# Optimization experiments

Measured on AMD Instinct MI355X. Metric: run time of the kernel, lower is better.

## Reference

```python
import jax, jax.numpy as jnp
import numpy as np
import math

HEADS = 4
LN_EPS = 1e-5


def _layer_norm(x, gamma, beta):
    # LayerNorm over last dim (N=4096), matching nn.LayerNorm(4096)
    mu = jnp.mean(x, axis=-1, keepdims=True)
    var = jnp.mean((x - mu) ** 2, axis=-1, keepdims=True)
    return (x - mu) * jax.lax.rsqrt(var + LN_EPS) * gamma + beta


def setup_inputs() -> dict:
    key = jax.random.key(0)
    ks = jax.random.split(key, 10)
    L, IMG, N = 1024, 1024, 4096
    s_img = 1.0 / math.sqrt(IMG)
    s_L = 1.0 / math.sqrt(L)
    return {
        "point_features": jax.random.normal(ks[0], (1, L, N), jnp.float32),
        "img_features": jax.random.normal(ks[1], (1, IMG, N), jnp.float32),
        # 4 per-head 1x1 convs IMG_chl -> L_chl
        "W_img": jax.random.normal(ks[2], (HEADS, L, IMG), jnp.float32) * s_img,
        "b_img": jax.random.normal(ks[3], (HEADS, L), jnp.float32) * s_img,
        # conv_L: L_chl -> L_chl
        "W_L": jax.random.normal(ks[4], (L, L), jnp.float32) * s_L,
        "b_L": jax.random.normal(ks[5], (L,), jnp.float32) * s_L,
        # LayerNorm(4096)
        "ln_g": jnp.ones((N,), jnp.float32),
        "ln_b": jnp.zeros((N,), jnp.float32),
        # conv_fusion: L_chl -> L_chl
        "W_f": jax.random.normal(ks[6], (L, L), jnp.float32) * s_L,
        "b_f": jax.random.normal(ks[7], (L,), jnp.float32) * s_L,
    }


def reference(point_features, img_features, W_img, b_img, W_L, b_L, ln_g, ln_b, W_f, b_f):
    # L_query = conv_L(point_features): [1, L, N]
    L_query = jnp.einsum('oi,bin->bon', W_L, point_features) + b_L[None, :, None]
    dk = L_query.shape[1]
    N = L_query.shape[2]

    # All 4 head keys at once: [H, 1, L, N]
    keys = jnp.einsum('hoi,bin->hbon', W_img, img_features) + b_img[:, None, :, None]

    # score_i = sum_c(key_i * query) / sqrt(dk)  -> cat over heads: [H, N] (B=1)
    score = jnp.sum(keys * L_query[None], axis=2).reshape(HEADS, N) / jnp.sqrt(jnp.float32(dk))

    # softmax across heads (dim=0), weightmap = [1, H, N]
    weight = jax.nn.softmax(score, axis=0)
    weightmap = weight[None]

    # z = sum_h weight[h] * key_h : [1, L, N]
    z = jnp.einsum('hn,hbcn->bcn', weight, keys)

    fused = _layer_norm(z + L_query, ln_g, ln_b)
    fusion_features = jnp.einsum('oi,bin->bon', W_f, fused) + b_f[None, :, None]
    return (fusion_features, weightmap)
```

## Files before the change

kernel.cpp:

```cpp
#include <hip/hip_runtime.h>
#include <hip/hip_bf16.h>
#include <stdint.h>

using u16 = unsigned short;

typedef __attribute__((ext_vector_type(8))) short bf16x8;
typedef __attribute__((ext_vector_type(4))) float f32x4;

typedef const __attribute__((address_space(1))) unsigned int* gas_t;
typedef __attribute__((address_space(3))) unsigned int* las_t;

__device__ inline void g2l16(const u16* g, u16* l) {
  __builtin_amdgcn_global_load_lds((gas_t)g, (las_t)l, 16, 0, 0);
}

__device__ inline u16 f2b(float x) {
  union { float f; uint32_t u; } v; v.f = x;
  uint32_t r = (v.u + 0x7FFFu + ((v.u >> 16) & 1u)) >> 16;
  return (u16)r;
}
__device__ inline float b2f(u16 b) {
  union { uint32_t u; float f; } v; v.u = ((uint32_t)b) << 16;
  return v.f;
}
__device__ inline float b2f_lo(uint32_t p) {
  union { uint32_t u; float f; } v; v.u = p << 16; return v.f;
}
__device__ inline float b2f_hi(uint32_t p) {
  union { uint32_t u; float f; } v; v.u = p & 0xFFFF0000u; return v.f;
}

__device__ inline void store_out(float* p, float v) { *p = v; }
__device__ inline void store_out(u16* p, float v) { *p = f2b(v); }

template<typename OutT>
__device__ inline void gemm_tile_128(const u16* __restrict__ A,
                                     const u16* __restrict__ Bt,
                                     const float* __restrict__ bias,
                                     OutT* __restrict__ C,
                                     int m0, int n0, int N, int K,
                                     u16* As, u16* Bs)
{
  const int tid  = threadIdx.x;
  const int wave = tid >> 6;
  const int lane = tid & 63;
  const int wm = wave >> 1, wn = wave & 1;
  const int lr = lane & 15;
  const int lq = lane >> 4;
  const int x7 = lr & 7;

  const int srow = tid >> 3;
  const int sgc  = (tid & 7) ^ (srow & 7);
  const u16* gA = A  + (size_t)(m0 + srow) * K + sgc * 8;
  const u16* gB = Bt + (size_t)(n0 + srow) * K + sgc * 8;
  u16* dstA = As + wave * 512;
  u16* dstB = Bs + wave * 512;

  f32x4 acc[4][4];
  #pragma unroll
  for (int i = 0; i < 4; ++i)
    #pragma unroll
    for (int j = 0; j < 4; ++j)
      acc[i][j] = (f32x4){0.f, 0.f, 0.f, 0.f};

  for (int k0 = 0; k0 < K; k0 += 64) {
    #pragma unroll
    for (int s = 0; s < 4; ++s) {
      g2l16(gA + (size_t)(s * 32) * K + k0, dstA + s * 2048);
      g2l16(gB + (size_t)(s * 32) * K + k0, dstB + s * 2048);
    }
    __syncthreads();

    #pragma unroll
    for (int ks = 0; ks < 2; ++ks) {
      const int pa = (ks * 4 + lq) ^ x7;
      bf16x8 af[4], bfr[4];
      #pragma unroll
      for (int im = 0; im < 4; ++im)
        af[im] = *(const bf16x8*)&As[(wm * 64 + im * 16 + lr) * 64 + pa * 8];
      #pragma unroll
      for (int in = 0; in < 4; ++in)
        bfr[in] = *(const bf16x8*)&Bs[(wn * 64 + in * 16 + lr) * 64 + pa * 8];

      #pragma unroll
      for (int im = 0; im < 4; ++im)
        #pragma unroll
        for (int in = 0; in < 4; ++in)
          acc[im][in] = __builtin_amdgcn_mfma_f32_16x16x32_bf16(
              af[im], bfr[in], acc[im][in], 0, 0, 0);
    }
    __syncthreads();
  }

  #pragma unroll
  for (int im = 0; im < 4; ++im) {
    const int mbase = m0 + wm * 64 + im * 16 + lq * 4;
    #pragma unroll
    for (int in = 0; in < 4; ++in) {
      const int ncol = n0 + wn * 64 + in * 16 + lr;
      #pragma unroll
      for (int r = 0; r < 4; ++r) {
        const int m = mbase + r;
        store_out(C + (size_t)m * N + ncol, acc[im][in][r] + bias[m]);
      }
    }
  }
}

__global__ __launch_bounds__(256)
void gemm_keys_q(const u16* __restrict__ WIb, const u16* __restrict__ IT,
                 const float* __restrict__ bim, u16* __restrict__ KEYS,
                 const u16* __restrict__ WLb, const u16* __restrict__ PT,
                 const float* __restrict__ bL, u16* __restrict__ Qb)
{
  __shared__ u16 As[128 * 64];
  __shared__ u16 Bs[128 * 64];
  const int by = blockIdx.y;
  const bool keys = (by < 32);
  const u16*   A    = keys ? WIb : WLb;
  const u16*   Bt   = keys ? IT  : PT;
  const float* bias = keys ? bim : bL;
  u16*         C    = keys ? KEYS : Qb;
  const int m0 = (by & 31) * 128;
  const int n0 = blockIdx.x * 128;
  gemm_tile_128<u16>(A, Bt, bias, C, m0, n0, 4096, 1024, As, Bs);
}

template<typename OutT>
__global__ __launch_bounds__(256)
void gemm_bt_64(const u16* __restrict__ A, const u16* __restrict__ Bt,
                const float* __restrict__ bias, OutT* __restrict__ C,
                int M, int N, int K)
{
  __shared__ u16 As[64 * 64];
  __shared__ u16 Bs[128 * 64];

  const int tid  = threadIdx.x;
  const int wave = tid >> 6;
  const int lane = tid & 63;
  const int lr = lane & 15;
  const int lq = lane >> 4;
  const int x7 = lr & 7;

  const int m0 = blockIdx.y * 64;
  const int n0 = blockIdx.x * 128;

  const int srow = tid >> 3;
  const int sgc  = (tid & 7) ^ (srow & 7);
  const u16* gA = A  + (size_t)(m0 + srow) * K + sgc * 8;
  const u16* gB = Bt + (size_t)(n0 + srow) * K + sgc * 8;
  u16* dstA = As + wave * 512;
  u16* dstB = Bs + wave * 512;

  f32x4 acc[4][2];
  #pragma unroll
  for (int i = 0; i < 4; ++i)
    #pragma unroll
    for (int j = 0; j < 2; ++j)
      acc[i][j] = (f32x4){0.f, 0.f, 0.f, 0.f};

  for (int k0 = 0; k0 < K; k0 += 64) {
    #pragma unroll
    for (int s = 0; s < 2; ++s)
      g2l16(gA + (size_t)(s * 32) * K + k0, dstA + s * 2048);
    #pragma unroll
    for (int s = 0; s < 4; ++s)
      g2l16(gB + (size_t)(s * 32) * K + k0, dstB + s * 2048);
    __syncthreads();

    #pragma unroll
    for (int ks = 0; ks < 2; ++ks) {
      const int pa = (ks * 4 + lq) ^ x7;
      bf16x8 af[4], bfr[2];
      #pragma unroll
      for (int im = 0; im < 4; ++im)
        af[im] = *(const bf16x8*)&As[(im * 16 + lr) * 64 + pa * 8];
      #pragma unroll
      for (int in = 0; in < 2; ++in)
        bfr[in] = *(const bf16x8*)&Bs[(wave * 32 + in * 16 + lr) * 64 + pa * 8];

      #pragma unroll
      for (int im = 0; im < 4; ++im)
        #pragma unroll
        for (int in = 0; in < 2; ++in)
          acc[im][in] = __builtin_amdgcn_mfma_f32_16x16x32_bf16(
              af[im], bfr[in], acc[im][in], 0, 0, 0);
    }
    __syncthreads();
  }

  #pragma unroll
  for (int im = 0; im < 4; ++im) {
    const int mbase = m0 + im * 16 + lq * 4;
    #pragma unroll
    for (int in = 0; in < 2; ++in) {
      const int ncol = n0 + wave * 32 + in * 16 + lr;
      #pragma unroll
      for (int r = 0; r < 4; ++r) {
        const int m = mbase + r;
        store_out(C + (size_t)m * N + ncol, acc[im][in][r] + bias[m]);
      }
    }
  }
}

__device__ inline void transpose_tile_f32(const float* __restrict__ in,
                                          u16* __restrict__ out,
                                          int R, int C, int r0, int c0)
{
  __shared__ u16 T[64 * 68];
  const int tr = (threadIdx.x >> 4) * 4;
  const int tc = (threadIdx.x & 15) * 4;
  float4 v[4];
  #pragma unroll
  for (int i = 0; i < 4; ++i)
    v[i] = *(const float4*)&in[(size_t)(r0 + tr + i) * C + c0 + tc];
  #pragma unroll
  for (int j = 0; j < 4; ++j) {
    ushort4 o;
    o.x = f2b(((const float*)&v[0])[j]);
    o.y = f2b(((const float*)&v[1])[j]);
    o.z = f2b(((const float*)&v[2])[j]);
    o.w = f2b(((const float*)&v[3])[j]);
    *(ushort4*)&T[(tc + j) * 68 + tr] = o;
  }
  __syncthreads();
  #pragma unroll
  for (int j = 0; j < 4; ++j) {
    const ushort4 o = *(const ushort4*)&T[(tr + j) * 68 + tc];
    *(ushort4*)&out[(size_t)(c0 + tr + j) * R + r0 + tc] = o;
  }
}

__device__ inline void transpose_tile_u16(const u16* __restrict__ in,
                                          u16* __restrict__ out,
                                          int R, int C, int r0, int c0)
{
  __shared__ u16 T[64 * 68];
  const int tr = (threadIdx.x >> 4) * 4;
  const int tc = (threadIdx.x & 15) * 4;
  ushort4 v[4];
  #pragma unroll
  for (int i = 0; i < 4; ++i)
    v[i] = *(const ushort4*)&in[(size_t)(r0 + tr + i) * C + c0 + tc];
  #pragma unroll
  for (int j = 0; j < 4; ++j) {
    ushort4 o;
    o.x = ((const u16*)&v[0])[j];
    o.y = ((const u16*)&v[1])[j];
    o.z = ((const u16*)&v[2])[j];
    o.w = ((const u16*)&v[3])[j];
    *(ushort4*)&T[(tc + j) * 68 + tr] = o;
  }
  __syncthreads();
  #pragma unroll
  for (int j = 0; j < 4; ++j) {
    const ushort4 o = *(const ushort4*)&T[(tr + j) * 68 + tc];
    *(ushort4*)&out[(size_t)(c0 + tr + j) * R + r0 + tc] = o;
  }
}

__global__ __launch_bounds__(256)
void prep(const float* __restrict__ P, u16* __restrict__ PT,
          const float* __restrict__ I, u16* __restrict__ IT,
          const float4* __restrict__ wim, const float4* __restrict__ wl,
          const float4* __restrict__ wf, ushort4* __restrict__ wimb,
          ushort4* __restrict__ wlb, ushort4* __restrict__ wfb,
          float4* __restrict__ score0)
{
  const int bid = blockIdx.x;
  if (bid < 2048) {
    const int z   = bid >> 10;
    const int rem = bid & 1023;
    const int c0  = (rem & 63) * 64;
    const int r0  = (rem >> 6) * 64;
    transpose_tile_f32(z ? I : P, z ? IT : PT, 1024, 4096, r0, c0);
  } else if (bid < 8192) {
    int i = (bid - 2048) * 256 + threadIdx.x;
    const float4* src; ushort4* dst;
    if (i < 1048576)      { src = wim; dst = wimb; }
    else if (i < 1310720) { src = wl;  dst = wlb;  i -= 1048576; }
    else                  { src = wf;  dst = wfb;  i -= 1310720; }
    const float4 v = src[i];
    ushort4 o;
    o.x = f2b(v.x); o.y = f2b(v.y); o.z = f2b(v.z); o.w = f2b(v.w);
    dst[i] = o;
  } else {
    const int i = (bid - 8192) * 256 + threadIdx.x;
    score0[i] = (float4){0.f, 0.f, 0.f, 0.f};
  }
}

__global__ __launch_bounds__(256)
void transpose_u16(const u16* __restrict__ in, u16* __restrict__ out)
{
  const int c0 = (blockIdx.x & 63) * 64;
  const int r0 = (blockIdx.x >> 6) * 64;
  transpose_tile_u16(in, out, 1024, 4096, r0, c0);
}

__global__ __launch_bounds__(256)
void score_partial(const u16* __restrict__ keys, const u16* __restrict__ Qb,
                   float* __restrict__ score)
{
  const int n  = (blockIdx.x * 256 + threadIdx.x) * 2;
  const int c0 = blockIdx.y * 16;
  float s0[4] = {0.f, 0.f, 0.f, 0.f};
  float s1[4] = {0.f, 0.f, 0.f, 0.f};
  for (int c = c0; c < c0 + 16; ++c) {
    const uint32_t qv = *(const uint32_t*)&Qb[(size_t)c * 4096 + n];
    const float q0 = b2f_lo(qv), q1 = b2f_hi(qv);
    #pragma unroll
    for (int h = 0; h < 4; ++h) {
      const uint32_t kv = *(const uint32_t*)&keys[((size_t)((h << 10) + c)) * 4096 + n];
      s0[h] = fmaf(q0, b2f_lo(kv), s0[h]);
      s1[h] = fmaf(q1, b2f_hi(kv), s1[h]);
    }
  }
  #pragma unroll
  for (int h = 0; h < 4; ++h) {
    atomicAdd(&score[h * 4096 + n],     s0[h] * 0.03125f);
    atomicAdd(&score[h * 4096 + n + 1], s1[h] * 0.03125f);
  }
}

__global__ __launch_bounds__(256)
void softmax_h(const float* __restrict__ score, float* __restrict__ wmap)
{
  const int n = blockIdx.x * 256 + threadIdx.x;
  const float s0 = score[n], s1 = score[4096 + n];
  const float s2 = score[8192 + n], s3 = score[12288 + n];
  const float m = fmaxf(fmaxf(s0, s1), fmaxf(s2, s3));
  const float e0 = expf(s0 - m), e1 = expf(s1 - m);
  const float e2 = expf(s2 - m), e3 = expf(s3 - m);
  const float inv = 1.f / (e0 + e1 + e2 + e3);
  wmap[n] = e0 * inv; wmap[4096 + n] = e1 * inv;
  wmap[8192 + n] = e2 * inv; wmap[12288 + n] = e3 * inv;
}

__global__ __launch_bounds__(256)
void z_ln(const u16* __restrict__ keys, const u16* __restrict__ Qb,
          const float* __restrict__ w, const float* __restrict__ g,
          const float* __restrict__ bb, u16* __restrict__ fused)
{
  const int c  = blockIdx.x;
  const int tx = threadIdx.x;
  float t[16];
  float s = 0.f, s2 = 0.f;
  #pragma unroll
  for (int j = 0; j < 2; ++j) {
    const int n = tx * 8 + j * 2048;
    const uint4 qv = *(const uint4*)&Qb[(size_t)c * 4096 + n];
    float z[8] = {0.f,0.f,0.f,0.f,0.f,0.f,0.f,0.f};
    #pragma unroll
    for (int h = 0; h < 4; ++h) {
      const uint4 kv = *(const uint4*)&keys[((size_t)((h << 10) + c)) * 4096 + n];
      const float4 w0 = *(const float4*)&w[h * 4096 + n];
      const float4 w1 = *(const float4*)&w[h * 4096 + n + 4];
      z[0] = fmaf(w0.x, b2f_lo(kv.x), z[0]);
      z[1] = fmaf(w0.y, b2f_hi(kv.x), z[1]);
      z[2] = fmaf(w0.z, b2f_lo(kv.y), z[2]);
      z[3] = fmaf(w0.w, b2f_hi(kv.y), z[3]);
      z[4] = fmaf(w1.x, b2f_lo(kv.z), z[4]);
      z[5] = fmaf(w1.y, b2f_hi(kv.z), z[5]);
      z[6] = fmaf(w1.z, b2f_lo(kv.w), z[6]);
      z[7] = fmaf(w1.w, b2f_hi(kv.w), z[7]);
    }
    const uint32_t qs[4] = {qv.x, qv.y, qv.z, qv.w};
    #pragma unroll
    for (int e = 0; e < 4; ++e) {
      const float v0 = z[2 * e]     + b2f_lo(qs[e]);
      const float v1 = z[2 * e + 1] + b2f_hi(qs[e]);
      t[8 * j + 2 * e]     = v0;
      t[8 * j + 2 * e + 1] = v1;
      s += v0 + v1;
      s2 = fmaf(v0, v0, fmaf(v1, v1, s2));
    }
  }
  #pragma unroll
  for (int o = 32; o > 0; o >>= 1) {
    s  += __shfl_down(s, o);
    s2 += __shfl_down(s2, o);
  }
  __shared__ float rbuf[8];
  const int wave = tx >> 6, lane = tx & 63;
  if (lane == 0) { rbuf[wave] = s; rbuf[4 + wave] = s2; }
  __syncthreads();
  s  = rbuf[0] + rbuf[1] + rbuf[2] + rbuf[3];
  s2 = rbuf[4] + rbuf[5] + rbuf[6] + rbuf[7];
  const float mu  = s * (1.f / 4096.f);
  const float var = s2 * (1.f / 4096.f) - mu * mu;
  const float rs  = rsqrtf(var + 1e-5f);
  #pragma unroll
  for (int j = 0; j < 2; ++j) {
    const int n = tx * 8 + j * 2048;
    #pragma unroll
    for (int q4 = 0; q4 < 2; ++q4) {
      const float4 gv = *(const float4*)&g[n + 4 * q4];
      const float4 bv = *(const float4*)&bb[n + 4 * q4];
      ushort4 o;
      o.x = f2b((t[8 * j + 4 * q4]     - mu) * rs * gv.x + bv.x);
      o.y = f2b((t[8 * j + 4 * q4 + 1] - mu) * rs * gv.y + bv.y);
      o.z = f2b((t[8 * j + 4 * q4 + 2] - mu) * rs * gv.z + bv.z);
      o.w = f2b((t[8 * j + 4 * q4 + 3] - mu) * rs * gv.w + bv.w);
      *(ushort4*)&fused[(size_t)c * 4096 + n + 4 * q4] = o;
    }
  }
}

extern "C" void kernel_launch(void* const* d_in, const int* in_sizes, int n_in,
                              void* d_out, int out_size, void* d_ws, size_t ws_size,
                              hipStream_t stream)
{
  const float* P   = (const float*)d_in[0];
  const float* I   = (const float*)d_in[1];
  const float* Wim = (const float*)d_in[2];
  const float* bim = (const float*)d_in[3];
  const float* WL  = (const float*)d_in[4];
  const float* bL  = (const float*)d_in[5];
  const float* lng = (const float*)d_in[6];
  const float* lnb = (const float*)d_in[7];
  const float* Wf  = (const float*)d_in[8];
  const float* bf_ = (const float*)d_in[9];
  float* out = (float*)d_out;

  char* ws = (char*)d_ws;
  u16*   PT     = (u16*)(ws + 0);
  u16*   IT     = (u16*)(ws + (size_t)8  * 1048576);
  u16*   WLb    = (u16*)(ws + (size_t)16 * 1048576);
  u16*   WIb    = (u16*)(ws + (size_t)18 * 1048576);
  u16*   WFb    = (u16*)(ws + (size_t)26 * 1048576);
  u16*   Qb     = (u16*)(ws + (size_t)28 * 1048576);
  u16*   KEYS   = (u16*)(ws + (size_t)36 * 1048576);
  float* SCORE  = (float*)(ws + (size_t)68 * 1048576);
  u16*   FUSED  = (u16*)(ws + (size_t)70 * 1048576);
  u16*   FUSEDT = (u16*)(ws + (size_t)78 * 1048576);

  const dim3 b256(256);

  prep<<<8208, b256, 0, stream>>>(P, PT, I, IT,
                                  (const float4*)Wim, (const float4*)WL,
                                  (const float4*)Wf, (ushort4*)WIb,
                                  (ushort4*)WLb, (ushort4*)WFb,
                                  (float4*)SCORE);

  gemm_keys_q<<<dim3(32, 40), b256, 0, stream>>>(WIb, IT, bim, KEYS,
                                                 WLb, PT, bL, Qb);

  score_partial<<<dim3(8, 64), b256, 0, stream>>>(KEYS, Qb, SCORE);
  float* wmap = out + (size_t)1024 * 4096;
  softmax_h<<<16, b256, 0, stream>>>(SCORE, wmap);

  z_ln<<<1024, b256, 0, stream>>>(KEYS, Qb, wmap, lng, lnb, FUSED);
  transpose_u16<<<1024, b256, 0, stream>>>(FUSED, FUSEDT);

  gemm_bt_64<float><<<dim3(32, 16), b256, 0, stream>>>(WFb, FUSEDT, bf_, out, 1024, 4096, 1024);
}
```

Before: 212.0 us.

## Fuse score, softmax, z+LayerNorm and transpose into one cooperative kernel

Four separate launches (score partials, head softmax, z+LayerNorm, bf16 transpose) become a single cooperative kernel of 1024 blocks, with grid-wide syncs between the stages. The aim is to remove three launch gaps and their tail idle time. In exchange it adds grid.sync barriers and needs all 1024 blocks resident at once (launch_bounds 256,4). The score stage also now does scalar 2-byte loads per thread, where it previously did paired 4-byte loads.

```diff
diff --git a/kernel.cpp b/kernel.cpp
--- a/kernel.cpp
+++ b/kernel.cpp
@@ -1,6 +1,9 @@
 #include <hip/hip_runtime.h>
 #include <hip/hip_bf16.h>
+#include <hip/hip_cooperative_groups.h>
 #include <stdint.h>
+
+namespace cg = cooperative_groups;
 
 using u16 = unsigned short;
 
@@ -291,121 +294,114 @@
   }
 }
 
-__global__ __launch_bounds__(256)
-void transpose_u16(const u16* __restrict__ in, u16* __restrict__ out)
-{
-  const int c0 = (blockIdx.x & 63) * 64;
-  const int r0 = (blockIdx.x >> 6) * 64;
-  transpose_tile_u16(in, out, 1024, 4096, r0, c0);
-}
-
-__global__ __launch_bounds__(256)
-void score_partial(const u16* __restrict__ keys, const u16* __restrict__ Qb,
-                   float* __restrict__ score)
-{
-  const int n  = (blockIdx.x * 256 + threadIdx.x) * 2;
-  const int c0 = blockIdx.y * 16;
-  float s0[4] = {0.f, 0.f, 0.f, 0.f};
-  float s1[4] = {0.f, 0.f, 0.f, 0.f};
-  for (int c = c0; c < c0 + 16; ++c) {
-    const uint32_t qv = *(const uint32_t*)&Qb[(size_t)c * 4096 + n];
-    const float q0 = b2f_lo(qv), q1 = b2f_hi(qv);
-    #pragma unroll
-    for (int h = 0; h < 4; ++h) {
-      const uint32_t kv = *(const uint32_t*)&keys[((size_t)((h << 10) + c)) * 4096 + n];
-      s0[h] = fmaf(q0, b2f_lo(kv), s0[h]);
-      s1[h] = fmaf(q1, b2f_hi(kv), s1[h]);
-    }
-  }
-  #pragma unroll
-  for (int h = 0; h < 4; ++h) {
-    atomicAdd(&score[h * 4096 + n],     s0[h] * 0.03125f);
-    atomicAdd(&score[h * 4096 + n + 1], s1[h] * 0.03125f);
-  }
-}
-
-__global__ __launch_bounds__(256)
-void softmax_h(const float* __restrict__ score, float* __restrict__ wmap)
-{
-  const int n = blockIdx.x * 256 + threadIdx.x;
-  const float s0 = score[n], s1 = score[4096 + n];
-  const float s2 = score[8192 + n], s3 = score[12288 + n];
-  const float m = fmaxf(fmaxf(s0, s1), fmaxf(s2, s3));
-  const float e0 = expf(s0 - m), e1 = expf(s1 - m);
-  const float e2 = expf(s2 - m), e3 = expf(s3 - m);
-  const float inv = 1.f / (e0 + e1 + e2 + e3);
-  wmap[n] = e0 * inv; wmap[4096 + n] = e1 * inv;
-  wmap[8192 + n] = e2 * inv; wmap[12288 + n] = e3 * inv;
-}
-
-__global__ __launch_bounds__(256)
-void z_ln(const u16* __restrict__ keys, const u16* __restrict__ Qb,
-          const float* __restrict__ w, const float* __restrict__ g,
-          const float* __restrict__ bb, u16* __restrict__ fused)
-{
-  const int c  = blockIdx.x;
+__global__ __launch_bounds__(256, 4)
+void attn_fused(const u16* __restrict__ keys, const u16* __restrict__ Qb,
+                float* __restrict__ score, float* __restrict__ wmap,
+                const float* __restrict__ g, const float* __restrict__ bb,
+                u16* __restrict__ fused, u16* __restrict__ fusedT)
+{
+  cg::grid_group grid = cg::this_grid();
+  const int b  = blockIdx.x;
   const int tx = threadIdx.x;
-  float t[16];
-  float s = 0.f, s2 = 0.f;
-  #pragma unroll
-  for (int j = 0; j < 2; ++j) {
-    const int n = tx * 8 + j * 2048;
-    const uint4 qv = *(const uint4*)&Qb[(size_t)c * 4096 + n];
-    float z[8] = {0.f,0.f,0.f,0.f,0.f,0.f,0.f,0.f};
-    #pragma unroll
-    for (int h = 0; h < 4; ++h) {
-      const uint4 kv = *(const uint4*)&keys[((size_t)((h << 10) + c)) * 4096 + n];
-      const float4 w0 = *(const float4*)&w[h * 4096 + n];
-      const float4 w1 = *(const float4*)&w[h * 4096 + n + 4];
-      z[0] = fmaf(w0.x, b2f_lo(kv.x), z[0]);
-      z[1] = fmaf(w0.y, b2f_hi(kv.x), z[1]);
-      z[2] = fmaf(w0.z, b2f_lo(kv.y), z[2]);
-      z[3] = fmaf(w0.w, b2f_hi(kv.y), z[3]);
-      z[4] = fmaf(w1.x, b2f_lo(kv.z), z[4]);
-      z[5] = fmaf(w1.y, b2f_hi(kv.z), z[5]);
-      z[6] = fmaf(w1.z, b2f_lo(kv.w), z[6]);
-      z[7] = fmaf(w1.w, b2f_hi(kv.w), z[7]);
-    }
-    const uint32_t qs[4] = {qv.x, qv.y, qv.z, qv.w};
-    #pragma unroll
-    for (int e = 0; e < 4; ++e) {
-      const float v0 = z[2 * e]     + b2f_lo(qs[e]);
-      const float v1 = z[2 * e + 1] + b2f_hi(qs[e]);
-      t[8 * j + 2 * e]     = v0;
-      t[8 * j + 2 * e + 1] = v1;
-      s += v0 + v1;
-      s2 = fmaf(v0, v0, fmaf(v1, v1, s2));
-    }
-  }
-  #pragma unroll
-  for (int o = 32; o > 0; o >>= 1) {
-    s  += __shfl_down(s, o);
-    s2 += __shfl_down(s2, o);
-  }
-  __shared__ float rbuf[8];
-  const int wave = tx >> 6, lane = tx & 63;
-  if (lane == 0) { rbuf[wave] = s; rbuf[4 + wave] = s2; }
-  __syncthreads();
-  s  = rbuf[0] + rbuf[1] + rbuf[2] + rbuf[3];
-  s2 = rbuf[4] + rbuf[5] + rbuf[6] + rbuf[7];
-  const float mu  = s * (1.f / 4096.f);
-  const float var = s2 * (1.f / 4096.f) - mu * mu;
-  const float rs  = rsqrtf(var + 1e-5f);
-  #pragma unroll
-  for (int j = 0; j < 2; ++j) {
-    const int n = tx * 8 + j * 2048;
-    #pragma unroll
-    for (int q4 = 0; q4 < 2; ++q4) {
-      const float4 gv = *(const float4*)&g[n + 4 * q4];
-      const float4 bv = *(const float4*)&bb[n + 4 * q4];
-      ushort4 o;
-      o.x = f2b((t[8 * j + 4 * q4]     - mu) * rs * gv.x + bv.x);
-      o.y = f2b((t[8 * j + 4 * q4 + 1] - mu) * rs * gv.y + bv.y);
-      o.z = f2b((t[8 * j + 4 * q4 + 2] - mu) * rs * gv.z + bv.z);
-      o.w = f2b((t[8 * j + 4 * q4 + 3] - mu) * rs * gv.w + bv.w);
-      *(ushort4*)&fused[(size_t)c * 4096 + n + 4 * q4] = o;
-    }
-  }
+
+  {
+    const int n  = (b & 31) * 128 + (tx & 127);
+    const int c0 = (b >> 5) * 32 + (tx >> 7) * 16;
+    float s[4] = {0.f, 0.f, 0.f, 0.f};
+    for (int c = c0; c < c0 + 16; ++c) {
+      const float q = b2f(Qb[(size_t)c * 4096 + n]);
+      #pragma unroll
+      for (int h = 0; h < 4; ++h)
+        s[h] = fmaf(q, b2f(keys[((size_t)((h << 10) + c)) * 4096 + n]), s[h]);
+    }
+    #pragma unroll
+    for (int h = 0; h < 4; ++h)
+      atomicAdd(&score[h * 4096 + n], s[h] * 0.03125f);
+  }
+  grid.sync();
+
+  if (b < 16) {
+    const int n = b * 256 + tx;
+    const float s0 = score[n], s1 = score[4096 + n];
+    const float s2 = score[8192 + n], s3 = score[12288 + n];
+    const float m = fmaxf(fmaxf(s0, s1), fmaxf(s2, s3));
+    const float e0 = expf(s0 - m), e1 = expf(s1 - m);
+    const float e2 = expf(s2 - m), e3 = expf(s3 - m);
+    const float inv = 1.f / (e0 + e1 + e2 + e3);
+    wmap[n] = e0 * inv; wmap[4096 + n] = e1 * inv;
+    wmap[8192 + n] = e2 * inv; wmap[12288 + n] = e3 * inv;
+  }
+  __threadfence();
+  grid.sync();
+
+  {
+    const int c = b;
+    float t[16];
+    float s = 0.f, s2 = 0.f;
+    #pragma unroll
+    for (int j = 0; j < 2; ++j) {
+      const int n = tx * 8 + j * 2048;
+      const uint4 qv = *(const uint4*)&Qb[(size_t)c * 4096 + n];
+      float z[8] = {0.f,0.f,0.f,0.f,0.f,0.f,0.f,0.f};
+      #pragma unroll
+      for (int h = 0; h < 4; ++h) {
+        const uint4 kv = *(const uint4*)&keys[((size_t)((h << 10) + c)) * 4096 + n];
+        const float4 w0 = *(const float4*)&wmap[h * 4096 + n];
+        const float4 w1 = *(const float4*)&wmap[h * 4096 + n + 4];
+        z[0] = fmaf(w0.x, b2f_lo(kv.x), z[0]);
+        z[1] = fmaf(w0.y, b2f_hi(kv.x), z[1]);
+        z[2] = fmaf(w0.z, b2f_lo(kv.y), z[2]);
+        z[3] = fmaf(w0.w, b2f_hi(kv.y), z[3]);
+        z[4] = fmaf(w1.x, b2f_lo(kv.z), z[4]);
+        z[5] = fmaf(w1.y, b2f_hi(kv.z), z[5]);
+        z[6] = fmaf(w1.z, b2f_lo(kv.w), z[6]);
+        z[7] = fmaf(w1.w, b2f_hi(kv.w), z[7]);
+      }
+      const uint32_t qs[4] = {qv.x, qv.y, qv.z, qv.w};
+      #pragma unroll
+      for (int e = 0; e < 4; ++e) {
+        const float v0 = z[2 * e]     + b2f_lo(qs[e]);
+        const float v1 = z[2 * e + 1] + b2f_hi(qs[e]);
+        t[8 * j + 2 * e]     = v0;
+        t[8 * j + 2 * e + 1] = v1;
+        s += v0 + v1;
+        s2 = fmaf(v0, v0, fmaf(v1, v1, s2));
+      }
+    }
+    #pragma unroll
+    for (int o = 32; o > 0; o >>= 1) {
+      s  += __shfl_down(s, o);
+      s2 += __shfl_down(s2, o);
+    }
+    __shared__ float rbuf[8];
+    const int wave = tx >> 6, lane = tx & 63;
+    if (lane == 0) { rbuf[wave] = s; rbuf[4 + wave] = s2; }
+    __syncthreads();
+    s  = rbuf[0] + rbuf[1] + rbuf[2] + rbuf[3];
+    s2 = rbuf[4] + rbuf[5] + rbuf[6] + rbuf[7];
+    const float mu  = s * (1.f / 4096.f);
+    const float var = s2 * (1.f / 4096.f) - mu * mu;
+    const float rs  = rsqrtf(var + 1e-5f);
+    #pragma unroll
+    for (int j = 0; j < 2; ++j) {
+      const int n = tx * 8 + j * 2048;
+      #pragma unroll
+      for (int q4 = 0; q4 < 2; ++q4) {
+        const float4 gv = *(const float4*)&g[n + 4 * q4];
+        const float4 bv = *(const float4*)&bb[n + 4 * q4];
+        ushort4 o;
+        o.x = f2b((t[8 * j + 4 * q4]     - mu) * rs * gv.x + bv.x);
+        o.y = f2b((t[8 * j + 4 * q4 + 1] - mu) * rs * gv.y + bv.y);
+        o.z = f2b((t[8 * j + 4 * q4 + 2] - mu) * rs * gv.z + bv.z);
+        o.w = f2b((t[8 * j + 4 * q4 + 3] - mu) * rs * gv.w + bv.w);
+        *(ushort4*)&fused[(size_t)c * 4096 + n + 4 * q4] = o;
+      }
+    }
+  }
+  __threadfence();
+  grid.sync();
+
+  transpose_tile_u16(fused, fusedT, 1024, 4096, (b >> 6) * 64, (b & 63) * 64);
 }
 
 extern "C" void kernel_launch(void* const* d_in, const int* in_sizes, int n_in,
@@ -447,12 +443,13 @@
   gemm_keys_q<<<dim3(32, 40), b256, 0, stream>>>(WIb, IT, bim, KEYS,
                                                  WLb, PT, bL, Qb);
 
-  score_partial<<<dim3(8, 64), b256, 0, stream>>>(KEYS, Qb, SCORE);
   float* wmap = out + (size_t)1024 * 4096;
-  softmax_h<<<16, b256, 0, stream>>>(SCORE, wmap);
-
-  z_ln<<<1024, b256, 0, stream>>>(KEYS, Qb, wmap, lng, lnb, FUSED);
-  transpose_u16<<<1024, b256, 0, stream>>>(FUSED, FUSEDT);
+  {
+    void* args[] = {(void*)&KEYS, (void*)&Qb, (void*)&SCORE, (void*)&wmap,
+                    (void*)&lng, (void*)&lnb, (void*)&FUSED, (void*)&FUSEDT};
+    hipLaunchCooperativeKernel((void*)attn_fused, dim3(1024), b256,
+                               args, 0, stream);
+  }
 
   gemm_bt_64<float><<<dim3(32, 16), b256, 0, stream>>>(WFb, FUSEDT, bf_, out, 1024, 4096, 1024);
 }
```

Measured after the change: 681.3 us. 3.21x slower.
